# Kernel optimization log

Measured on AMD Instinct MI355X. Metric: run time of the kernel, lower is better.

Reference implementation:

```python
import jax, jax.numpy as jnp
import numpy as np

NUM_HEADS = 8
NUM_LAYERS = 4
BASE_THR = 0.5     # AdaptiveLIF base_threshold (state reset -> no adaptation on single step)
TAU_MEM = 5.0      # tau_mem (single step from zero state: mem = decay*0 + x = x)
SURR_SLOPE = 5.0   # fast-sigmoid surrogate slope (forward path unaffected)
EPS = 1e-5
NEG = -1e9


@jax.custom_vjp
def spike(u):
    return (u > 0.0).astype(u.dtype)

def _spike_fwd(u):
    return (u > 0.0).astype(u.dtype), u

def _spike_bwd(u, g):
    return (g / (1.0 + SURR_SLOPE * jnp.abs(u)) ** 2,)

spike.defvjp(_spike_fwd, _spike_bwd)


def lif(x):
    # AdaptiveLIF, single timestep from reset state: mem = x, thr = base_threshold
    return spike(x - BASE_THR)


def layer_norm(x, g, b):
    m = jnp.mean(x, axis=-1, keepdims=True)
    v = jnp.mean((x - m) ** 2, axis=-1, keepdims=True)
    return (x - m) * jax.lax.rsqrt(v + EPS) * g + b


def dsa(x, wq, bq, wk, bk, wv, bv, wo, bo, top_k):
    # Dynamic Sparse Attention: dense scores -> per-query top-k mask -> softmax -> AV
    B, T, D = x.shape
    H = NUM_HEADS
    dh = D // H

    def heads(w, bias):
        return (x @ w.T + bias).reshape(B, T, H, dh).transpose(0, 2, 1, 3)  # [B,H,T,dh]

    q, k, v = heads(wq, bq), heads(wk, bk), heads(wv, bv)
    scores = jnp.einsum('bhqd,bhkd->bhqk', q, k) / jnp.sqrt(jnp.asarray(dh, x.dtype))
    vals, idx = jax.lax.top_k(scores, top_k)  # [B,H,T,K]

    # scatter top-k values into a -inf-filled score matrix (exact top-k sparsity)
    N = B * H * T
    rows = jnp.arange(N)[:, None]
    sp = jnp.full((N, T), NEG, scores.dtype).at[rows, idx.reshape(N, top_k)].set(vals.reshape(N, top_k))
    attn = jax.nn.softmax(sp.reshape(B, H, T, T), axis=-1)

    out = jnp.einsum('bhqk,bhkd->bhqd', attn, v)
    out = out.transpose(0, 2, 1, 3).reshape(B, T, D)
    out = out @ wo.T + bo
    return lif(out)  # spiking output of attention


def ffn(x, w1, b1, w2, b2):
    h = lif(x @ w1.T + b1)
    return lif(h @ w2.T + b2)


def setup_inputs() -> dict:
    key = jax.random.key(0)
    ks = jax.random.split(key, 16)
    L, D, F, IN, OUT, B, T = NUM_LAYERS, 512, 2048, 128, 256, 2, 2048
    s = 0.02
    return {
        'x': jax.random.normal(ks[0], (B, T, IN), jnp.float32),
        'emb_w': jax.random.normal(ks[1], (D, IN), jnp.float32) * s,
        'emb_b': jnp.zeros((D,), jnp.float32),
        'pos_emb': jax.random.normal(ks[2], (1, T, D), jnp.float32) * s,
        'wq': jax.random.normal(ks[3], (L, D, D), jnp.float32) * s,
        'bq': jnp.zeros((L, D), jnp.float32),
        'wk': jax.random.normal(ks[4], (L, D, D), jnp.float32) * s,
        'bk': jnp.zeros((L, D), jnp.float32),
        'wv': jax.random.normal(ks[5], (L, D, D), jnp.float32) * s,
        'bv': jnp.zeros((L, D), jnp.float32),
        'wo': jax.random.normal(ks[6], (L, D, D), jnp.float32) * s,
        'bo': jnp.zeros((L, D), jnp.float32),
        'ln1_g': jnp.ones((L, D), jnp.float32),
        'ln1_b': jnp.zeros((L, D), jnp.float32),
        'fc1_w': jax.random.normal(ks[7], (L, F, D), jnp.float32) * s,
        'fc1_b': jnp.zeros((L, F), jnp.float32),
        'fc2_w': jax.random.normal(ks[8], (L, D, F), jnp.float32) * s,
        'fc2_b': jnp.zeros((L, D), jnp.float32),
        'ln2_g': jnp.ones((L, D), jnp.float32),
        'ln2_b': jnp.zeros((L, D), jnp.float32),
        'fnorm_g': jnp.ones((D,), jnp.float32),
        'fnorm_b': jnp.zeros((D,), jnp.float32),
        'cls_w': jax.random.normal(ks[9], (OUT, D), jnp.float32) * s,
        'cls_b': jnp.zeros((OUT,), jnp.float32),
        'top_k': 32,
    }


def reference(x, emb_w, emb_b, pos_emb, wq, bq, wk, bk, wv, bv, wo, bo,
              ln1_g, ln1_b, fc1_w, fc1_b, fc2_w, fc2_b, ln2_g, ln2_b,
              fnorm_g, fnorm_b, cls_w, cls_b, top_k):
    B, T, _ = x.shape
    h = x @ emb_w.T + emb_b + pos_emb[:, :T, :]
    for l in range(NUM_LAYERS):
        a = dsa(h, wq[l], bq[l], wk[l], bk[l], wv[l], bv[l], wo[l], bo[l], top_k)
        h = layer_norm(h + a, ln1_g[l], ln1_b[l])
        f = ffn(h, fc1_w[l], fc1_b[l], fc2_w[l], fc2_b[l])
        h = layer_norm(h + f, ln2_g[l], ln2_b[l])
    h = layer_norm(h, fnorm_g, fnorm_b)
    pooled = jnp.mean(h, axis=1)  # [B, D]
    return pooled @ cls_w.T + cls_b
```

## Files before the change

kernel.cpp:

```cpp
#include <hip/hip_runtime.h>
#include <math.h>
#include <float.h>

#define T_SEQ  2048
#define DMODEL 512
#define NHEAD  8
#define DHEAD  64
#define FDIM   2048
#define NLAYER 4
#define NB     2
#define MROWS  (NB*T_SEQ)

typedef _Float16 f16x8 __attribute__((ext_vector_type(8)));
typedef float    f32x4 __attribute__((ext_vector_type(4)));

__device__ __forceinline__ void async16(const _Float16* g, _Float16* l) {
    __builtin_amdgcn_global_load_lds(
        (const __attribute__((address_space(1))) unsigned int*)g,
        (__attribute__((address_space(3))) unsigned int*)l, 16, 0, 0);
}

template<int BN, int EPI>
__global__ __launch_bounds__(256) void gemm_k(
    const float* __restrict__ A, const float* __restrict__ W,
    const float* __restrict__ bias, const float* __restrict__ pos,
    float* __restrict__ C, int M, int N, int K)
{
    constexpr int BM = 128;
    constexpr int BK = 32;
    constexpr int MN = BN / 16;
    __shared__ float As[BK][BM + 4];
    __shared__ float Ws[BK][BN + 4];
    const int tid = threadIdx.x;
    const int n0 = blockIdx.x * BN;
    const int m0 = blockIdx.y * BM;
    const int tx = tid & 15;
    const int ty = tid >> 4;

    float acc[8][MN];
    #pragma unroll
    for (int i = 0; i < 8; ++i)
        #pragma unroll
        for (int j = 0; j < MN; ++j) acc[i][j] = 0.f;

    for (int k0 = 0; k0 < K; k0 += BK) {
        #pragma unroll
        for (int it = 0; it < 4; ++it) {
            int qq = tid + 256 * it;
            int m = qq >> 3, kq = qq & 7;
            float4 v4 = *(const float4*)(A + (size_t)(m0 + m) * K + k0 + kq * 4);
            As[kq*4+0][m] = v4.x; As[kq*4+1][m] = v4.y;
            As[kq*4+2][m] = v4.z; As[kq*4+3][m] = v4.w;
        }
        #pragma unroll
        for (int it = 0; it < BN/32; ++it) {
            int qq = tid + 256 * it;
            int n = qq >> 3, kq = qq & 7;
            float4 v4 = *(const float4*)(W + (size_t)(n0 + n) * K + k0 + kq * 4);
            Ws[kq*4+0][n] = v4.x; Ws[kq*4+1][n] = v4.y;
            Ws[kq*4+2][n] = v4.z; Ws[kq*4+3][n] = v4.w;
        }
        __syncthreads();
        for (int kk = 0; kk < BK; ++kk) {
            float a[8], b[MN];
            float4 a0 = *(const float4*)&As[kk][ty*8];
            float4 a1 = *(const float4*)&As[kk][ty*8+4];
            a[0]=a0.x; a[1]=a0.y; a[2]=a0.z; a[3]=a0.w;
            a[4]=a1.x; a[5]=a1.y; a[6]=a1.z; a[7]=a1.w;
            float4 b0 = *(const float4*)&Ws[kk][tx*4];
            b[0]=b0.x; b[1]=b0.y; b[2]=b0.z; b[3]=b0.w;
            if constexpr (MN == 8) {
                float4 b1 = *(const float4*)&Ws[kk][64 + tx*4];
                b[4]=b1.x; b[5]=b1.y; b[6]=b1.z; b[7]=b1.w;
            }
            #pragma unroll
            for (int i = 0; i < 8; ++i)
                #pragma unroll
                for (int j = 0; j < MN; ++j)
                    acc[i][j] = fmaf(a[i], b[j], acc[i][j]);
        }
        __syncthreads();
    }

    #pragma unroll
    for (int i = 0; i < 8; ++i) {
        int m = m0 + ty*8 + i;
        #pragma unroll
        for (int jb = 0; jb < MN/4; ++jb) {
            int nn = n0 + jb*64 + tx*4;
            float4 r;
            r.x = acc[i][jb*4+0] + bias[nn+0];
            r.y = acc[i][jb*4+1] + bias[nn+1];
            r.z = acc[i][jb*4+2] + bias[nn+2];
            r.w = acc[i][jb*4+3] + bias[nn+3];
            if constexpr (EPI == 1) {
                const float* pp = pos + (size_t)(m & (T_SEQ-1)) * DMODEL + nn;
                r.x += pp[0]; r.y += pp[1]; r.z += pp[2]; r.w += pp[3];
            }
            *(float4*)(C + (size_t)m * N + nn) = r;
        }
    }
}

template<int BM, int BN, int ASRC, int EPI, int LAYOUT>
__global__ __launch_bounds__(256, (BM == 64) ? 3 : 2) void mgemm_k(
    const _Float16* __restrict__ AH, const _Float16* __restrict__ AL,
    const _Float16* __restrict__ WH, const _Float16* __restrict__ WL,
    const float* __restrict__ bias,
    float* __restrict__ O0, float* __restrict__ O1, float* __restrict__ O2,
    float* __restrict__ O3, float* __restrict__ O4,
    int M, int N, int K)
{
    constexpr int MI = BM / 32;
    constexpr int NJ = BN / 32;
    __shared__ _Float16 AsH[2][4][BM][8];
    __shared__ _Float16 AsL[(ASRC == 0) ? 2 : 1][(ASRC == 0) ? 4 : 1][(ASRC == 0) ? BM : 1][8];
    __shared__ _Float16 WsH[2][4][BN][8];
    __shared__ _Float16 WsL[2][4][BN][8];

    const int tid = threadIdx.x;
    const int npan = N / BN;
    const int bid  = blockIdx.x;
    const int n0 = (bid % npan) * BN;
    const int m0 = (bid / npan) * BM;
    const int wv = tid >> 6, lane = tid & 63;
    const int mw = (wv >> 1) * (BM/2), nw = (wv & 1) * (BN/2);
    const int fr = lane & 15;
    const int kb = lane >> 4;

    const int wsrow = tid >> 1;
    const int wskb  = (tid & 1) * 2;
    const int wkoff = (tid & 1) * 16;
    const int arow  = tid >> 2, akb = tid & 3;

    f16x8 pa0, pa1, pal0, pal1;

    auto stageW = [&](int k0, int buf) {
        const size_t base = ((size_t)((k0 >> 3) + wv) * N + n0) * 8;
        const _Float16* sH = WH + base + (size_t)lane * 8;
        const _Float16* sL = WL + base + (size_t)lane * 8;
        async16(sH, &WsH[buf][wv][0][0]);
        async16(sL, &WsL[buf][wv][0][0]);
        if constexpr (BN == 128) {
            async16(sH + 512, &WsH[buf][wv][64][0]);
            async16(sL + 512, &WsL[buf][wv][64][0]);
        }
    };
    auto gloadA = [&](int k0) {
        if constexpr (BM == 128) {
            const _Float16* ap = AH + (size_t)(m0 + wsrow) * K + k0 + wkoff;
            pa0 = *(const f16x8*)ap;
            pa1 = *(const f16x8*)(ap + 8);
            if constexpr (ASRC == 0) {
                const _Float16* alp = AL + (size_t)(m0 + wsrow) * K + k0 + wkoff;
                pal0 = *(const f16x8*)alp;
                pal1 = *(const f16x8*)(alp + 8);
            }
        } else {
            pa0 = *(const f16x8*)(AH + (size_t)(m0 + arow) * K + k0 + akb*8);
            if constexpr (ASRC == 0)
                pal0 = *(const f16x8*)(AL + (size_t)(m0 + arow) * K + k0 + akb*8);
        }
    };
    auto swriteA = [&](int buf) {
        if constexpr (BM == 128) {
            *(f16x8*)&AsH[buf][wskb  ][wsrow][0] = pa0;
            *(f16x8*)&AsH[buf][wskb+1][wsrow][0] = pa1;
            if constexpr (ASRC == 0) {
                *(f16x8*)&AsL[buf][wskb  ][wsrow][0] = pal0;
                *(f16x8*)&AsL[buf][wskb+1][wsrow][0] = pal1;
            }
        } else {
            *(f16x8*)&AsH[buf][akb][arow][0] = pa0;
            if constexpr (ASRC == 0)
                *(f16x8*)&AsL[buf][akb][arow][0] = pal0;
        }
    };

    f32x4 acc[MI][NJ];
    #pragma unroll
    for (int i = 0; i < MI; ++i)
        #pragma unroll
        for (int j = 0; j < NJ; ++j) acc[i][j] = (f32x4)(0.f);

    const int NT = K >> 5;
    int cur = 0;
    stageW(0, 0);
    gloadA(0);
    swriteA(0);
    __syncthreads();

    for (int t = 0; t < NT; ++t) {
        const bool more = (t + 1 < NT);
        if (more) {
            stageW((t + 1) << 5, cur ^ 1);
            gloadA((t + 1) << 5);
        }

        f16x8 aH[MI], aL[MI], bH[NJ], bL[NJ];
        #pragma unroll
        for (int i = 0; i < MI; ++i) {
            aH[i] = *(const f16x8*)&AsH[cur][kb][mw + i*16 + fr][0];
            if constexpr (ASRC == 0) aL[i] = *(const f16x8*)&AsL[cur][kb][mw + i*16 + fr][0];
        }
        #pragma unroll
        for (int j = 0; j < NJ; ++j) {
            bH[j] = *(const f16x8*)&WsH[cur][kb][nw + j*16 + fr][0];
            bL[j] = *(const f16x8*)&WsL[cur][kb][nw + j*16 + fr][0];
        }
        #pragma unroll
        for (int i = 0; i < MI; ++i)
            #pragma unroll
            for (int j = 0; j < NJ; ++j) {
                acc[i][j] = __builtin_amdgcn_mfma_f32_16x16x32_f16(aH[i], bH[j], acc[i][j], 0, 0, 0);
                acc[i][j] = __builtin_amdgcn_mfma_f32_16x16x32_f16(aH[i], bL[j], acc[i][j], 0, 0, 0);
                if constexpr (ASRC == 0)
                    acc[i][j] = __builtin_amdgcn_mfma_f32_16x16x32_f16(aL[i], bH[j], acc[i][j], 0, 0, 0);
            }
        if (more) {
            swriteA(cur ^ 1);
            __syncthreads();
            cur ^= 1;
        }
    }

    const int qq = lane >> 4;
    #pragma unroll
    for (int j = 0; j < NJ; ++j) {
        int n = n0 + nw + j*16 + fr;
        float bv = bias[n];
        #pragma unroll
        for (int i = 0; i < MI; ++i) {
            #pragma unroll
            for (int r = 0; r < 4; ++r) {
                int m = m0 + mw + i*16 + qq*4 + r;
                float val = acc[i][j][r] * (1.f/1024.f) + bv;
                if constexpr (EPI == 2) val = val > 0.5f ? 1.f : 0.f;
                if constexpr (EPI == 3) {
                    ((_Float16*)O0)[(size_t)m * N + n] = (val > 0.5f) ? (_Float16)16.f : (_Float16)0.f;
                } else if constexpr (LAYOUT == 0) {
                    O0[(size_t)m * N + n] = val;
                } else {
                    int b_ = m >> 11, t_ = m & (T_SEQ-1);
                    if (n < 512) {
                        size_t hl = (((size_t)(b_*NHEAD + (n>>6))*T_SEQ + t_) << 6) + (n & 63);
                        float s16 = 16.f * val;
                        _Float16 hh = (_Float16)s16;
                        ((_Float16*)O0)[hl] = hh;
                        ((_Float16*)O1)[hl] = (_Float16)(s16 - (float)hh);
                    } else if (n < 1024) {
                        int nn = n - 512;
                        size_t hl = (((size_t)(b_*NHEAD + (nn>>6))*T_SEQ + t_) << 6) + (nn & 63);
                        float s16 = 16.f * val;
                        _Float16 hh = (_Float16)s16;
                        ((_Float16*)O2)[hl] = hh;
                        ((_Float16*)O3)[hl] = (_Float16)(s16 - (float)hh);
                    } else {
                        int nn = n - 1024;
                        O4[(((size_t)(b_*NHEAD + (nn>>6))*T_SEQ + t_) << 6) + (nn & 63)] = val;
                    }
                }
            }
        }
    }
}

__global__ __launch_bounds__(256) void cvtw_k(
    const float* __restrict__ w, _Float16* __restrict__ H, _Float16* __restrict__ L,
    int n, float scale)
{
    int i = blockIdx.x * 256 + threadIdx.x;
    if (i < n) {
        float s = scale * w[i];
        _Float16 h = (_Float16)s;
        H[i] = h;
        L[i] = (_Float16)(s - (float)h);
    }
}

__global__ __launch_bounds__(256) void cvtlayer_k(
    const float* __restrict__ wq, const float* __restrict__ wk, const float* __restrict__ wv,
    const float* __restrict__ bq, const float* __restrict__ bk, const float* __restrict__ bv,
    const float* __restrict__ wo, const float* __restrict__ f1w, const float* __restrict__ f2w,
    _Float16* __restrict__ WcatH, _Float16* __restrict__ WcatL, float* __restrict__ bcat,
    _Float16* __restrict__ WoH, _Float16* __restrict__ WoL,
    _Float16* __restrict__ W1H, _Float16* __restrict__ W1L,
    _Float16* __restrict__ W2H, _Float16* __restrict__ W2L)
{
    int i = blockIdx.x * 256 + threadIdx.x;
    float w;
    _Float16 *H, *L;
    int off;
    if (i < 786432) {
        int j = i;
        int kbq = j / 12288;
        int rem = j - kbq * 12288;
        int n = rem >> 3;
        int k = kbq * 8 + (j & 7);
        int sm = n >> 9, nn = n & 511;
        w = (sm == 0 ? wq : (sm == 1 ? wk : wv))[nn * 512 + k];
        H = WcatH; L = WcatL; off = j;
    } else if (i < 1048576) {
        int j = i - 786432;
        int kbq = j >> 12;
        int n = (j >> 3) & 511;
        int k = (kbq << 3) | (j & 7);
        w = wo[n * 512 + k];
        H = WoH; L = WoL; off = j;
    } else if (i < 2097152) {
        int j = i - 1048576;
        int kbq = j >> 14;
        int n = (j >> 3) & 2047;
        int k = (kbq << 3) | (j & 7);
        w = f1w[n * 512 + k];
        H = W1H; L = W1L; off = j;
    } else if (i < 3145728) {
        int j = i - 2097152;
        int kbq = j >> 12;
        int n = (j >> 3) & 511;
        int k = (kbq << 3) | (j & 7);
        w = f2w[n * 2048 + k];
        H = W2H; L = W2L; off = j;
    } else if (i < 3145728 + 1536) {
        int j = i - 3145728;
        int src = j >> 9, o = j & 511;
        bcat[j] = (src == 0 ? bq : (src == 1 ? bk : bv))[o];
        return;
    } else return;
    float s = 64.f * w;
    _Float16 h = (_Float16)s;
    H[off] = h;
    L[off] = (_Float16)(s - (float)h);
}

__global__ __launch_bounds__(512, 4) void attn_k(
    const _Float16* __restrict__ qH, const _Float16* __restrict__ qL,
    const _Float16* __restrict__ kH, const _Float16* __restrict__ kL,
    const float* __restrict__ v,
    _Float16* __restrict__ outH, _Float16* __restrict__ outL)
{
    __shared__ unsigned char lds[66560];
    _Float16* ksH = (_Float16*)(lds);
    _Float16* ksL = (_Float16*)(lds + 16384);
    float    (*ss)[132] = (float(*)[132])(lds + 32768);
    float*   wrow       = (float*)(lds + 32768);
    int*     irow       = (int*)(lds + 32768 + 8448);

    const int tid = threadIdx.x;
    const int bh  = blockIdx.y;
    const int t0  = blockIdx.x * 64;
    const _Float16* qHb = qH + ((size_t)bh * T_SEQ + t0) * DHEAD;
    const _Float16* qLb = qL + ((size_t)bh * T_SEQ + t0) * DHEAD;
    const _Float16* kHb = kH + (size_t)bh * T_SEQ * DHEAD;
    const _Float16* kLb = kL + (size_t)bh * T_SEQ * DHEAD;
    const float*    vb  = v  + (size_t)bh * T_SEQ * DHEAD;

    unsigned kreg[32];
    #pragma unroll
    for (int i = 0; i < 32; ++i) kreg[i] = 0u;

    const int wv = tid >> 6, lane = tid & 63;
    const int fr = lane & 15, q4 = lane >> 4;
    const int mh  = (wv >> 2) * 32;
    const int c0w = (wv & 3) * 32;
    const int srow = tid >> 3;
    const int ssub = tid & 7;

    f16x8 qaH[2][2], qaL[2][2];
    #pragma unroll
    for (int ks = 0; ks < 2; ++ks) {
        const int doff = ks*32 + q4*8;
        qaH[ks][0] = *(const f16x8*)(qHb + (mh + fr)*DHEAD + doff);
        qaH[ks][1] = *(const f16x8*)(qHb + (mh + 16 + fr)*DHEAD + doff);
        qaL[ks][0] = *(const f16x8*)(qLb + (mh + fr)*DHEAD + doff);
        qaL[ks][1] = *(const f16x8*)(qLb + (mh + 16 + fr)*DHEAD + doff);
    }

    auto stage = [&](int jt) {
        const int j0 = jt * 128;
        #pragma unroll
        for (int i = 0; i < 2; ++i) {
            const int r0 = wv*16 + i*8;
            const int cc = r0 + (lane >> 3);
            const int ch = (lane & 7) ^ (cc & 7);
            const size_t goff = (size_t)(j0 + cc) * DHEAD + ch*8;
            async16(kHb + goff, ksH + r0*64);
            async16(kLb + goff, ksL + r0*64);
        }
    };

    stage(0);
    __syncthreads();

    for (int jt = 0; jt < 16; ++jt) {
        const int j0 = jt * 128;

        f32x4 acc[2][2];
        acc[0][0] = (f32x4)(0.f); acc[0][1] = (f32x4)(0.f);
        acc[1][0] = (f32x4)(0.f); acc[1][1] = (f32x4)(0.f);
        #pragma unroll
        for (int ks = 0; ks < 2; ++ks) {
            const int chq  = ks*4 + q4;
            #pragma unroll
            for (int nj = 0; nj < 2; ++nj) {
                const int cc = c0w + nj*16 + fr;
                const int sl = cc*64 + (chq ^ (cc & 7))*8;
                f16x8 bHf = *(const f16x8*)&ksH[sl];
                f16x8 bLf = *(const f16x8*)&ksL[sl];
                acc[0][nj] = __builtin_amdgcn_mfma_f32_16x16x32_f16(qaH[ks][0], bHf, acc[0][nj], 0, 0, 0);
                acc[0][nj] = __builtin_amdgcn_mfma_f32_16x16x32_f16(qaH[ks][0], bLf, acc[0][nj], 0, 0, 0);
                acc[0][nj] = __builtin_amdgcn_mfma_f32_16x16x32_f16(qaL[ks][0], bHf, acc[0][nj], 0, 0, 0);
                acc[1][nj] = __builtin_amdgcn_mfma_f32_16x16x32_f16(qaH[ks][1], bHf, acc[1][nj], 0, 0, 0);
                acc[1][nj] = __builtin_amdgcn_mfma_f32_16x16x32_f16(qaH[ks][1], bLf, acc[1][nj], 0, 0, 0);
                acc[1][nj] = __builtin_amdgcn_mfma_f32_16x16x32_f16(qaL[ks][1], bHf, acc[1][nj], 0, 0, 0);
            }
        }
        #pragma unroll
        for (int mi = 0; mi < 2; ++mi)
            #pragma unroll
            for (int nj = 0; nj < 2; ++nj)
                #pragma unroll
                for (int r = 0; r < 4; ++r)
                    ss[mh + mi*16 + q4*4 + r][c0w + nj*16 + fr] = acc[mi][nj][r] * (1.f/2048.f);
        __syncthreads();

        if (jt < 15) stage(jt + 1);

        float4 c4[4];
        {
            const float* ssr = &ss[srow][0] + ssub*4;
            #pragma unroll
            for (int g = 0; g < 4; ++g) c4[g] = *(const float4*)(ssr + g*32);
        }
        unsigned cand[16];
        #pragma unroll
        for (int g = 0; g < 4; ++g) {
            float vg[4] = {c4[g].x, c4[g].y, c4[g].z, c4[g].w};
            #pragma unroll
            for (int r = 0; r < 4; ++r) {
                unsigned u = __float_as_uint(vg[r]);
                u ^= (unsigned)((int)u >> 31) | 0x80000000u;
                int col = ssub*4 + g*32 + r;
                cand[g*4+r] = (u & 0xFFFFF800u) | (unsigned)(2047 - (j0 + col));
            }
        }
        #pragma unroll
        for (int k2 = 2; k2 <= 16; k2 <<= 1) {
            #pragma unroll
            for (int j2 = k2 >> 1; j2 > 0; j2 >>= 1) {
                #pragma unroll
                for (int i2 = 0; i2 < 16; ++i2) {
                    int l2 = i2 ^ j2;
                    if (l2 > i2) {
                        unsigned a = cand[i2], b = cand[l2];
                        unsigned mn = a < b ? a : b;
                        unsigned mx = a < b ? b : a;
                        if ((i2 & k2) == 0) { cand[i2] = mx; cand[l2] = mn; }
                        else                { cand[i2] = mn; cand[l2] = mx; }
                    }
                }
            }
        }
        #pragma unroll
        for (int j2 = 0; j2 < 16; ++j2) {
            unsigned b = cand[15 - j2];
            if (kreg[16 + j2] < b) kreg[16 + j2] = b;
        }
        #pragma unroll
        for (int st = 16; st >= 1; st >>= 1) {
            #pragma unroll
            for (int i2 = 0; i2 < 32; ++i2) {
                if ((i2 & st) == 0) {
                    unsigned lo = kreg[i2], hi = kreg[i2 | st];
                    kreg[i2]      = lo < hi ? hi : lo;
                    kreg[i2 | st] = lo < hi ? lo : hi;
                }
            }
        }
        __syncthreads();
    }

    #pragma unroll
    for (int s = 1; s <= 4; s <<= 1) {
        #pragma unroll
        for (int i = 0; i < 16; ++i) {
            unsigned pa = (unsigned)__shfl_xor((int)kreg[31-i], s, 64);
            unsigned pb = (unsigned)__shfl_xor((int)kreg[i],    s, 64);
            if (pa > kreg[i])    kreg[i]    = pa;
            if (pb > kreg[31-i]) kreg[31-i] = pb;
        }
        #pragma unroll
        for (int st = 16; st >= 1; st >>= 1) {
            #pragma unroll
            for (int i2 = 0; i2 < 32; ++i2) {
                if ((i2 & st) == 0) {
                    unsigned lo = kreg[i2], hi = kreg[i2 | st];
                    kreg[i2]      = lo < hi ? hi : lo;
                    kreg[i2 | st] = lo < hi ? lo : hi;
                }
            }
        }
    }

    if (ssub == 0) {
        float w[32];
        #pragma unroll
        for (int i = 0; i < 32; ++i) {
            unsigned um = kreg[i] & 0xFFFFF800u;
            unsigned ub = (um & 0x80000000u) ? (um ^ 0x80000000u) : ~um;
            w[i] = __uint_as_float(ub);
        }
        float m = w[0];
        float s = 0.f;
        #pragma unroll
        for (int i = 0; i < 32; ++i) { w[i] = __expf(w[i] - m); s += w[i]; }
        float inv = 1.f / s;
        #pragma unroll
        for (int i = 0; i < 32; ++i) {
            wrow[srow*33 + i] = w[i] * inv;
            irow[srow*33 + i] = 2047 - (int)(kreg[i] & 0x7FFu);
        }
    }
    __syncthreads();

    const int wid = tid >> 6, lane2 = tid & 63;
    const int b = bh >> 3, h = bh & 7;
    for (int rr = wid; rr < 64; rr += 8) {
        float a0 = 0.f, a1 = 0.f, a2 = 0.f, a3 = 0.f;
        #pragma unroll
        for (int i = 0; i < 8; ++i) {
            a0 = fmaf(wrow[rr*33 + i],      vb[(size_t)irow[rr*33 + i]      * DHEAD + lane2], a0);
            a1 = fmaf(wrow[rr*33 + 8 + i],  vb[(size_t)irow[rr*33 + 8 + i]  * DHEAD + lane2], a1);
            a2 = fmaf(wrow[rr*33 + 16 + i], vb[(size_t)irow[rr*33 + 16 + i] * DHEAD + lane2], a2);
            a3 = fmaf(wrow[rr*33 + 24 + i], vb[(size_t)irow[rr*33 + 24 + i] * DHEAD + lane2], a3);
        }
        float accv = (a0 + a1) + (a2 + a3);
        size_t oi = ((size_t)(b * T_SEQ + t0 + rr)) * DMODEL + h * DHEAD + lane2;
        float s16 = 16.f * accv;
        _Float16 hh = (_Float16)s16;
        outH[oi] = hh;
        outL[oi] = (_Float16)(s16 - (float)hh);
    }
}

__global__ __launch_bounds__(256) void ln_k(
    const float* __restrict__ x, const float* __restrict__ res,
    const float* __restrict__ g, const float* __restrict__ bb,
    float* __restrict__ out, _Float16* __restrict__ oH, _Float16* __restrict__ oL)
{
    __shared__ float red[8];
    const int row = blockIdx.x;
    const int tid = threadIdx.x;
    const float* xr = x + (size_t)row * DMODEL;
    float v0 = xr[tid], v1 = xr[tid + 256];
    if (res) {
        const float* rr = res + (size_t)row * DMODEL;
        v0 += rr[tid]; v1 += rr[tid + 256];
    }
    float s = v0 + v1;
    #pragma unroll
    for (int o = 1; o < 64; o <<= 1) s += __shfl_xor(s, o);
    const int wid = tid >> 6, lane = tid & 63;
    if (lane == 0) red[wid] = s;
    __syncthreads();
    float mean = (red[0] + red[1] + red[2] + red[3]) * (1.f / DMODEL);
    float d0 = v0 - mean, d1 = v1 - mean;
    float qs = d0*d0 + d1*d1;
    #pragma unroll
    for (int o = 1; o < 64; o <<= 1) qs += __shfl_xor(qs, o);
    if (lane == 0) red[4 + wid] = qs;
    __syncthreads();
    float var = (red[4] + red[5] + red[6] + red[7]) * (1.f / DMODEL);
    float rs = rsqrtf(var + 1e-5f);
    float o0 = d0 * rs * g[tid]       + bb[tid];
    float o1 = d1 * rs * g[tid + 256] + bb[tid + 256];
    size_t base = (size_t)row * DMODEL;
    out[base + tid]       = o0;
    out[base + tid + 256] = o1;
    float s0 = 16.f * o0, s1 = 16.f * o1;
    _Float16 h0 = (_Float16)s0, h1 = (_Float16)s1;
    oH[base + tid]       = h0;
    oH[base + tid + 256] = h1;
    oL[base + tid]       = (_Float16)(s0 - (float)h0);
    oL[base + tid + 256] = (_Float16)(s1 - (float)h1);
}

__global__ __launch_bounds__(256) void pool_k(
    const float* __restrict__ h, float* __restrict__ part)
{
    const int chunk = blockIdx.x & 15;
    const int idx = (blockIdx.x >> 4) * 256 + threadIdx.x;
    const int b = idx >> 9, d = idx & 511;
    const float* p = h + ((size_t)b * T_SEQ + chunk * 128) * DMODEL + d;
    float s = 0.f;
    for (int t = 0; t < 128; ++t) s += p[(size_t)t * DMODEL];
    part[chunk * 1024 + idx] = s;
}

__global__ __launch_bounds__(256) void poolsum_k(
    const float* __restrict__ part, float* __restrict__ pooled)
{
    int idx = blockIdx.x * 256 + threadIdx.x;
    float s = 0.f;
    #pragma unroll
    for (int c = 0; c < 16; ++c) s += part[c * 1024 + idx];
    pooled[idx] = s * (1.f / T_SEQ);
}

__global__ __launch_bounds__(256) void cls_k(
    const float* __restrict__ pooled, const float* __restrict__ w,
    const float* __restrict__ bias, float* __restrict__ out)
{
    const int wid = threadIdx.x >> 6, lane = threadIdx.x & 63;
    const int oi = blockIdx.x * 4 + wid;
    const int b = oi >> 8, o = oi & 255;
    const float* pr = pooled + b * DMODEL;
    const float* wr = w + (size_t)o * DMODEL;
    float s = 0.f;
    for (int d = lane; d < DMODEL; d += 64) s = fmaf(pr[d], wr[d], s);
    #pragma unroll
    for (int off = 1; off < 64; off <<= 1) s += __shfl_xor(s, off);
    if (lane == 0) out[oi] = s + bias[o];
}

extern "C" void kernel_launch(void* const* d_in, const int* in_sizes, int n_in,
                              void* d_out, int out_size, void* d_ws, size_t ws_size,
                              hipStream_t stream)
{
    const float* x     = (const float*)d_in[0];
    const float* emb_w = (const float*)d_in[1];
    const float* emb_b = (const float*)d_in[2];
    const float* pos   = (const float*)d_in[3];
    const float* wq    = (const float*)d_in[4];
    const float* bq    = (const float*)d_in[5];
    const float* wk    = (const float*)d_in[6];
    const float* bk    = (const float*)d_in[7];
    const float* wv    = (const float*)d_in[8];
    const float* bv    = (const float*)d_in[9];
    const float* wo    = (const float*)d_in[10];
    const float* bo    = (const float*)d_in[11];
    const float* ln1g  = (const float*)d_in[12];
    const float* ln1b  = (const float*)d_in[13];
    const float* fc1w  = (const float*)d_in[14];
    const float* fc1b  = (const float*)d_in[15];
    const float* fc2w  = (const float*)d_in[16];
    const float* fc2b  = (const float*)d_in[17];
    const float* ln2g  = (const float*)d_in[18];
    const float* ln2b  = (const float*)d_in[19];
    const float* fng   = (const float*)d_in[20];
    const float* fnb   = (const float*)d_in[21];
    const float* clsw  = (const float*)d_in[22];
    const float* clsb  = (const float*)d_in[23];

    float* ws = (float*)d_ws;
    const size_t SZ  = (size_t)MROWS * DMODEL;
    const size_t HP  = SZ / 2;
    float*     h     = ws;
    float*     t1    = ws + 1*SZ;
    _Float16*  hH    = (_Float16*)(ws + 2*SZ);
    _Float16*  hL    = (_Float16*)(ws + 2*SZ + HP);
    _Float16*  aoH   = (_Float16*)(ws + 3*SZ);
    _Float16*  aoL   = (_Float16*)(ws + 3*SZ + HP);
    _Float16*  qbH   = (_Float16*)(ws + 4*SZ);
    _Float16*  qbL   = (_Float16*)(ws + 4*SZ + HP);
    _Float16*  kbH   = (_Float16*)(ws + 5*SZ);
    _Float16*  kbL   = (_Float16*)(ws + 5*SZ + HP);
    float*     vbuf  = ws + 6*SZ;
    _Float16*  WcatH = (_Float16*)(ws + 7*SZ);
    _Float16*  WcatL = (_Float16*)(ws + 7*SZ + 393216);
    _Float16*  WoH   = (_Float16*)(ws + 7*SZ + 786432);
    _Float16*  WoL   = (_Float16*)(ws + 7*SZ + 917504);
    _Float16*  W1H   = (_Float16*)(ws + 7*SZ + 1048576);
    _Float16*  W1L   = (_Float16*)(ws + 7*SZ + 1572864);
    _Float16*  W2H   = (_Float16*)(ws + 7*SZ + 2097152);
    _Float16*  W2L   = (_Float16*)(ws + 7*SZ + 2621440);
    float*     bcat  = ws + 7*SZ + 3145728;
    float*     pooled= ws + 7*SZ + 3145728 + 1536;
    float*     part  = ws + 7*SZ + 3145728 + 1536 + 1024;
    _Float16*  hid   = (_Float16*)(ws + 4*SZ);
    const size_t needed = (7*SZ + 3145728 + 1536 + 1024 + 16384) * sizeof(float);
    if (ws_size < needed) return;

    dim3 blk(256);

    gemm_k<64,1><<<dim3(DMODEL/64, MROWS/128), blk, 0, stream>>>(
        x, emb_w, emb_b, pos, h, MROWS, DMODEL, 128);
    cvtw_k<<<dim3((int)(SZ/256)), blk, 0, stream>>>(h, hH, hL, (int)SZ, 16.f);

    for (int l = 0; l < NLAYER; ++l) {
        const float* wq_l = wq + (size_t)l*DMODEL*DMODEL;
        const float* bq_l = bq + (size_t)l*DMODEL;
        const float* wk_l = wk + (size_t)l*DMODEL*DMODEL;
        const float* bk_l = bk + (size_t)l*DMODEL;
        const float* wv_l = wv + (size_t)l*DMODEL*DMODEL;
        const float* bv_l = bv + (size_t)l*DMODEL;
        const float* wo_l = wo + (size_t)l*DMODEL*DMODEL;
        const float* bo_l = bo + (size_t)l*DMODEL;
        const float* f1w_l = fc1w + (size_t)l*FDIM*DMODEL;
        const float* f1b_l = fc1b + (size_t)l*FDIM;
        const float* f2w_l = fc2w + (size_t)l*DMODEL*FDIM;
        const float* f2b_l = fc2b + (size_t)l*DMODEL;

        cvtlayer_k<<<dim3(12294), blk, 0, stream>>>(
            wq_l, wk_l, wv_l, bq_l, bk_l, bv_l, wo_l, f1w_l, f2w_l,
            WcatH, WcatL, bcat, WoH, WoL, W1H, W1L, W2H, W2L);

        mgemm_k<64,128,0,0,2><<<dim3(768), blk, 0, stream>>>(
            hH, hL, WcatH, WcatL, bcat,
            (float*)qbH, (float*)qbL, (float*)kbH, (float*)kbL, vbuf,
            MROWS, 1536, DMODEL);

        attn_k<<<dim3(T_SEQ/64, NB*NHEAD), dim3(512), 0, stream>>>(
            qbH, qbL, kbH, kbL, vbuf, aoH, aoL);

        mgemm_k<64,64,0,2,0><<<dim3(512), blk, 0, stream>>>(
            aoH, aoL, WoH, WoL, bo_l, t1, nullptr, nullptr, nullptr, nullptr,
            MROWS, DMODEL, DMODEL);
        ln_k<<<dim3(MROWS), blk, 0, stream>>>(h, t1, ln1g + (size_t)l*DMODEL,
                                              ln1b + (size_t)l*DMODEL, h, hH, hL);

        mgemm_k<128,128,0,3,0><<<dim3(512), blk, 0, stream>>>(
            hH, hL, W1H, W1L, f1b_l, (float*)hid, nullptr, nullptr, nullptr, nullptr,
            MROWS, FDIM, DMODEL);
        mgemm_k<64,64,1,2,0><<<dim3(512), blk, 0, stream>>>(
            hid, nullptr, W2H, W2L, f2b_l, t1, nullptr, nullptr, nullptr, nullptr,
            MROWS, DMODEL, FDIM);
        ln_k<<<dim3(MROWS), blk, 0, stream>>>(h, t1, ln2g + (size_t)l*DMODEL,
                                              ln2b + (size_t)l*DMODEL, h, hH, hL);
    }

    ln_k<<<dim3(MROWS), blk, 0, stream>>>(h, nullptr, fng, fnb, h, hH, hL);
    pool_k<<<dim3(64), blk, 0, stream>>>(h, part);
    poolsum_k<<<dim3(4), blk, 0, stream>>>(part, pooled);
    cls_k<<<dim3(128), blk, 0, stream>>>(pooled, clsw, clsb, (float*)d_out);
}
```

Before: 1.094 ms.

## Run split-fp16 MFMA GEMMs with 8 waves per block instead of 4

Reworks the mgemm kernel to launch 512 threads (8 wavefronts) per block, splitting the output tile across more waves so each holds fewer accumulators. The loads are redistributed too: high and low weight halves are staged by different wave groups, and A-tile loads are split across thread halves. The aim is more latency hiding and fewer registers per wave. In exchange it adds block-level sync overhead, more LDS pressure per block, and smaller per-wave MFMA tiles.

Result: faster. 1.062 ms (-2.9%).

```diff
diff --git a/kernel.cpp b/kernel.cpp
--- a/kernel.cpp
+++ b/kernel.cpp
@@ -102,8 +102,8 @@
     }
 }
 
-template<int BM, int BN, int ASRC, int EPI, int LAYOUT>
-__global__ __launch_bounds__(256, (BM == 64) ? 3 : 2) void mgemm_k(
+template<int BM, int BN, int ASRC, int EPI, int LAYOUT, int MW>
+__global__ __launch_bounds__(512, MW) void mgemm_k(
     const _Float16* __restrict__ AH, const _Float16* __restrict__ AL,
     const _Float16* __restrict__ WH, const _Float16* __restrict__ WL,
     const float* __restrict__ bias,
@@ -111,8 +111,10 @@
     float* __restrict__ O3, float* __restrict__ O4,
     int M, int N, int K)
 {
-    constexpr int MI = BM / 32;
-    constexpr int NJ = BN / 32;
+    constexpr int WMv = (BM == 128) ? 4 : ((BN == 128) ? 2 : 4);
+    constexpr int WNv = 8 / WMv;
+    constexpr int MI  = BM / WMv / 16;
+    constexpr int NJ  = BN / WNv / 16;
     __shared__ _Float16 AsH[2][4][BM][8];
     __shared__ _Float16 AsL[(ASRC == 0) ? 2 : 1][(ASRC == 0) ? 4 : 1][(ASRC == 0) ? BM : 1][8];
     __shared__ _Float16 WsH[2][4][BN][8];
@@ -124,56 +126,52 @@
     const int n0 = (bid % npan) * BN;
     const int m0 = (bid / npan) * BM;
     const int wv = tid >> 6, lane = tid & 63;
-    const int mw = (wv >> 1) * (BM/2), nw = (wv & 1) * (BN/2);
+    const int mw = (wv / WNv) * (BM / WMv);
+    const int nw = (wv % WNv) * (BN / WNv);
     const int fr = lane & 15;
     const int kb = lane >> 4;
 
-    const int wsrow = tid >> 1;
-    const int wskb  = (tid & 1) * 2;
-    const int wkoff = (tid & 1) * 16;
-    const int arow  = tid >> 2, akb = tid & 3;
-
-    f16x8 pa0, pa1, pal0, pal1;
+    f16x8 pa0, pal0;
 
     auto stageW = [&](int k0, int buf) {
-        const size_t base = ((size_t)((k0 >> 3) + wv) * N + n0) * 8;
-        const _Float16* sH = WH + base + (size_t)lane * 8;
-        const _Float16* sL = WL + base + (size_t)lane * 8;
-        async16(sH, &WsH[buf][wv][0][0]);
-        async16(sL, &WsL[buf][wv][0][0]);
-        if constexpr (BN == 128) {
-            async16(sH + 512, &WsH[buf][wv][64][0]);
-            async16(sL + 512, &WsL[buf][wv][64][0]);
-        }
+        const int kb_ = wv & 3;
+        const _Float16* WP = (wv >= 4) ? WL : WH;
+        _Float16* db = (wv >= 4) ? &WsL[buf][kb_][0][0] : &WsH[buf][kb_][0][0];
+        const size_t sb = ((size_t)((k0 >> 3) + kb_) * N + n0);
+        async16(WP + (sb + lane) * 8, db);
+        if constexpr (BN == 128)
+            async16(WP + (sb + 64 + lane) * 8, db + 64 * 8);
     };
     auto gloadA = [&](int k0) {
         if constexpr (BM == 128) {
-            const _Float16* ap = AH + (size_t)(m0 + wsrow) * K + k0 + wkoff;
-            pa0 = *(const f16x8*)ap;
-            pa1 = *(const f16x8*)(ap + 8);
+            const int r_ = tid >> 2, kb_ = tid & 3;
+            pa0 = *(const f16x8*)(AH + (size_t)(m0 + r_) * K + k0 + kb_*8);
+            if constexpr (ASRC == 0)
+                pal0 = *(const f16x8*)(AL + (size_t)(m0 + r_) * K + k0 + kb_*8);
+        } else {
+            const int slot = tid & 255, r_ = slot >> 2, kb_ = slot & 3;
             if constexpr (ASRC == 0) {
-                const _Float16* alp = AL + (size_t)(m0 + wsrow) * K + k0 + wkoff;
-                pal0 = *(const f16x8*)alp;
-                pal1 = *(const f16x8*)(alp + 8);
-            }
-        } else {
-            pa0 = *(const f16x8*)(AH + (size_t)(m0 + arow) * K + k0 + akb*8);
-            if constexpr (ASRC == 0)
-                pal0 = *(const f16x8*)(AL + (size_t)(m0 + arow) * K + k0 + akb*8);
+                const _Float16* src = (tid < 256) ? AH : AL;
+                pa0 = *(const f16x8*)(src + (size_t)(m0 + r_) * K + k0 + kb_*8);
+            } else {
+                if (tid < 256)
+                    pa0 = *(const f16x8*)(AH + (size_t)(m0 + r_) * K + k0 + kb_*8);
+            }
         }
     };
     auto swriteA = [&](int buf) {
         if constexpr (BM == 128) {
-            *(f16x8*)&AsH[buf][wskb  ][wsrow][0] = pa0;
-            *(f16x8*)&AsH[buf][wskb+1][wsrow][0] = pa1;
+            *(f16x8*)&AsH[buf][tid & 3][tid >> 2][0] = pa0;
+            if constexpr (ASRC == 0)
+                *(f16x8*)&AsL[buf][tid & 3][tid >> 2][0] = pal0;
+        } else {
+            const int slot = tid & 255, r_ = slot >> 2, kb_ = slot & 3;
             if constexpr (ASRC == 0) {
-                *(f16x8*)&AsL[buf][wskb  ][wsrow][0] = pal0;
-                *(f16x8*)&AsL[buf][wskb+1][wsrow][0] = pal1;
-            }
-        } else {
-            *(f16x8*)&AsH[buf][akb][arow][0] = pa0;
-            if constexpr (ASRC == 0)
-                *(f16x8*)&AsL[buf][akb][arow][0] = pal0;
+                _Float16* d = (tid < 256) ? &AsH[buf][kb_][r_][0] : &AsL[buf][kb_][r_][0];
+                *(f16x8*)d = pa0;
+            } else {
+                if (tid < 256) *(f16x8*)&AsH[buf][kb_][r_][0] = pa0;
+            }
         }
     };
 
@@ -705,7 +703,7 @@
             wq_l, wk_l, wv_l, bq_l, bk_l, bv_l, wo_l, f1w_l, f2w_l,
             WcatH, WcatL, bcat, WoH, WoL, W1H, W1L, W2H, W2L);
 
-        mgemm_k<64,128,0,0,2><<<dim3(768), blk, 0, stream>>>(
+        mgemm_k<64,128,0,0,2,6><<<dim3(768), dim3(512), 0, stream>>>(
             hH, hL, WcatH, WcatL, bcat,
             (float*)qbH, (float*)qbL, (float*)kbH, (float*)kbL, vbuf,
             MROWS, 1536, DMODEL);
@@ -713,16 +711,16 @@
         attn_k<<<dim3(T_SEQ/64, NB*NHEAD), dim3(512), 0, stream>>>(
             qbH, qbL, kbH, kbL, vbuf, aoH, aoL);
 
-        mgemm_k<64,64,0,2,0><<<dim3(512), blk, 0, stream>>>(
+        mgemm_k<64,64,0,2,0,4><<<dim3(512), dim3(512), 0, stream>>>(
             aoH, aoL, WoH, WoL, bo_l, t1, nullptr, nullptr, nullptr, nullptr,
             MROWS, DMODEL, DMODEL);
         ln_k<<<dim3(MROWS), blk, 0, stream>>>(h, t1, ln1g + (size_t)l*DMODEL,
                                               ln1b + (size_t)l*DMODEL, h, hH, hL);
 
-        mgemm_k<128,128,0,3,0><<<dim3(512), blk, 0, stream>>>(
+        mgemm_k<128,128,0,3,0,4><<<dim3(512), dim3(512), 0, stream>>>(
             hH, hL, W1H, W1L, f1b_l, (float*)hid, nullptr, nullptr, nullptr, nullptr,
             MROWS, FDIM, DMODEL);
-        mgemm_k<64,64,1,2,0><<<dim3(512), blk, 0, stream>>>(
+        mgemm_k<64,64,1,2,0,4><<<dim3(512), dim3(512), 0, stream>>>(
             hid, nullptr, W2H, W2L, f2b_l, t1, nullptr, nullptr, nullptr, nullptr,
             MROWS, DMODEL, FDIM);
         ln_k<<<dim3(MROWS), blk, 0, stream>>>(h, t1, ln2g + (size_t)l*DMODEL,
```
